# Kernel tuning notes

Hardware: AMD Instinct MI355X
Metric: run time of the kernel (lower is better)

The kernel has to match this reference:

```python
import jax, jax.numpy as jnp
import numpy as np

PAD = 1
K = 3  # kernel_size


def conv2d(x, w, b):
    y = jax.lax.conv_general_dilated(
        x, w, window_strides=(1, 1), padding=((PAD, PAD), (PAD, PAD)),
        dimension_numbers=("NCHW", "OIHW", "NCHW"))
    return y + b[None, :, None, None]


def deform_conv2d(x, offset, weight, bias):
    # torchvision.ops.deform_conv2d semantics (stride=1, dilation=1, 1 offset group)
    B, C, H, W = x.shape
    O = weight.shape[0]
    K2 = K * K
    off = offset.reshape(B, K2, 2, H, W)  # [...,0]=dy, [...,1]=dx
    ky, kx = jnp.meshgrid(jnp.arange(K), jnp.arange(K), indexing="ij")
    ky = ky.reshape(K2).astype(x.dtype)
    kx = kx.reshape(K2).astype(x.dtype)
    hh = jnp.arange(H, dtype=x.dtype)
    ww = jnp.arange(W, dtype=x.dtype)
    # sampling coords, shape [B, K2, H, W]
    py = off[:, :, 0] + ky[None, :, None, None] + hh[None, None, :, None] - PAD
    px = off[:, :, 1] + kx[None, :, None, None] + ww[None, None, None, :] - PAD

    y0 = jnp.floor(py)
    x0 = jnp.floor(px)
    wy = (py - y0)[:, None]  # [B,1,K2,H,W]
    wx = (px - x0)[:, None]

    xf = x.reshape(B, C, H * W)

    def gather(iy, ix):
        valid = (iy >= 0) & (iy < H) & (ix >= 0) & (ix < W)
        iyc = jnp.clip(iy, 0, H - 1).astype(jnp.int32)
        ixc = jnp.clip(ix, 0, W - 1).astype(jnp.int32)
        idx = (iyc * W + ixc).reshape(B, 1, K2 * H * W)
        v = jnp.take_along_axis(xf, idx, axis=2).reshape(B, C, K2, H, W)
        return v * valid.reshape(B, 1, K2, H, W).astype(x.dtype)

    v00 = gather(y0, x0)
    v01 = gather(y0, x0 + 1)
    v10 = gather(y0 + 1, x0)
    v11 = gather(y0 + 1, x0 + 1)
    sampled = (v00 * (1 - wy) * (1 - wx) + v01 * (1 - wy) * wx
               + v10 * wy * (1 - wx) + v11 * wy * wx)  # [B,C,K2,H,W]
    out = jnp.einsum("bckhw,ock->bohw", sampled, weight.reshape(O, C, K2))
    return out + bias[None, :, None, None]


def setup_inputs() -> dict:
    key = jax.random.key(0)
    k1, k2, k3, k4, k5 = jax.random.split(key, 5)
    B, C, H, W = 4, 64, 192, 192
    O = 64
    x = jax.random.normal(k1, (B, C, H, W), dtype=jnp.float32)
    w_off = jax.random.normal(k2, (2 * K * K, C, K, K), dtype=jnp.float32) * 0.05
    b_off = jnp.zeros((2 * K * K,), dtype=jnp.float32)
    w_conv = jax.random.normal(k3, (O, C, K, K), dtype=jnp.float32) * (1.0 / np.sqrt(C * K * K))
    b_conv = jax.random.normal(k4, (O,), dtype=jnp.float32) * 0.01
    return {"x": x, "w_off": w_off, "b_off": b_off, "w_conv": w_conv, "b_conv": b_conv}


def reference(x, w_off, b_off, w_conv, b_conv):
    offset = conv2d(x, w_off, b_off)
    y = deform_conv2d(x, offset, w_conv, b_conv)
    return conv2d(y, w_conv, b_conv)  # module reuses self.conv on deform output
```

## Files before the change

### kernel.cpp

```cpp
#include <hip/hip_runtime.h>

constexpr int B = 4;
constexpr int C = 64;
constexpr int O = 64;
constexpr int OOFF = 18;
constexpr int H = 192;
constexpr int W = 192;

typedef __attribute__((ext_vector_type(8))) short short8;
typedef __attribute__((ext_vector_type(4))) float float4v;
typedef __attribute__((ext_vector_type(2))) float f32x2;
typedef __attribute__((ext_vector_type(2))) uint u32x2;
typedef __attribute__((ext_vector_type(2))) __bf16 bf16x2;

__device__ inline ushort f2bf(float f) {
  return __builtin_bit_cast(ushort, (__bf16)f);
}
__device__ inline uint pk2bf(float lo, float hi) {
  bf16x2 v;
  v.x = (__bf16)lo;
  v.y = (__bf16)hi;
  return __builtin_bit_cast(uint, v);
}
__device__ inline f32x2 upk(uint u) {
  u32x2 t;
  t.x = u << 16;
  t.y = u & 0xffff0000u;
  return __builtin_bit_cast(f32x2, t);
}

__global__ __launch_bounds__(256) void k_pre(const float* __restrict__ x,
                                             ushort* __restrict__ xtb,
                                             const float* __restrict__ w_conv,
                                             ushort* __restrict__ wBf,
                                             const float* __restrict__ w_off,
                                             ushort* __restrict__ wOf) {
  __shared__ float tile[64][17];
  const int bid = blockIdx.x;
  const int tid = threadIdx.x;
  if (bid < 9216) {
    const int w0 = (bid % 12) * 16;
    const int h = (bid / 12) % 192;
    const int b = bid / 2304;
    const int wl = tid & 15;
    const int c0 = tid >> 4;
#pragma unroll
    for (int r = 0; r < 4; ++r) {
      const int c = c0 + r * 16;
      tile[c][wl] = x[(((size_t)b * C + c) * H + h) * W + w0 + wl];
    }
    __syncthreads();
    const int c = tid & 63;
    const int qq = tid >> 6;
#pragma unroll
    for (int r = 0; r < 4; ++r) {
      const int wq = qq + r * 4;
      xtb[(((size_t)b * H + h) * W + w0 + wq) * C + c] = f2bf(tile[c][wq]);
    }
  } else if (bid < 9360) {
    const int i = (bid - 9216) * 256 + tid;
    const int j = i & 7;
    const int lane = (i >> 3) & 63;
    const int nt = (i >> 9) & 3;
    const int kstep = (i >> 11) & 1;
    const int kk = i >> 12;
    const int n = nt + 4 * (lane & 15);
    const int c = kstep * 32 + ((lane >> 4) & 3) * 8 + j;
    wBf[i] = f2bf(w_conv[((size_t)n * C + c) * 9 + kk]);
  } else {
    const int i = (bid - 9360) * 256 + tid;
    const int j = i & 7;
    const int lane = (i >> 3) & 63;
    const int nt = (i >> 9) & 1;
    const int ks = (i >> 10) & 1;
    const int kk = i >> 11;
    const int n = nt * 16 + (lane & 15);
    const int c = ks * 32 + ((lane >> 4) & 3) * 8 + j;
    wOf[i] = (n < OOFF) ? f2bf(w_off[((size_t)n * C + c) * 9 + kk]) : (ushort)0;
  }
}

__global__ __launch_bounds__(128) void k_fused(
    const ushort* __restrict__ xtb, const ushort* __restrict__ wOf,
    const float* __restrict__ b_off, const ushort* __restrict__ wBf,
    const float* __restrict__ b_conv, ushort* __restrict__ yt) {
  __shared__ ushort sA[2][2][64][8];
  __shared__ __align__(16) float offBuf[2][16][20];

  const int bid = blockIdx.x;
  const int xcd = bid & 7;
  const int s0 = bid >> 3;
  const int b = xcd >> 1;
  const int half = xcd & 1;
  const int th = s0 / 24;
  const int tw = s0 % 24;

  const int tid = threadIdx.x;
  const int wave = tid >> 6, lane = tid & 63;
  const int h0 = half * 96 + th * 4 + wave * 2;
  const int w0 = tw * 8;

  const int col = lane & 15, quad = lane >> 4;
  const int p = lane >> 2, qtr = lane & 3;
  const int prow = p >> 3, pcol = p & 7;
  const int h = h0 + prow, w = w0 + pcol;

  {
    float4v oacc[2];
#pragma unroll
    for (int nt = 0; nt < 2; ++nt) oacc[nt] = (float4v){0.f, 0.f, 0.f, 0.f};

    short8 oafr[2][2];

    auto oload = [&](int kk, int pb) {
      const int ky = kk / 3, kx = kk % 3;
      const int hh = h0 + (col >> 3) + ky - 1;
      const int ww = w0 + (col & 7) + kx - 1;
      const bool ok = ((unsigned)hh < (unsigned)H) && ((unsigned)ww < (unsigned)W);
      const int hhc = min(max(hh, 0), H - 1);
      const int wwc = min(max(ww, 0), W - 1);
      const ushort* pa = xtb + (((size_t)b * H + hhc) * W + wwc) * C + quad * 8;
#pragma unroll
      for (int ks = 0; ks < 2; ++ks) {
        short8 v = (short8)0;
        if (ok) v = *(const short8*)(pa + ks * 32);
        oafr[pb][ks] = v;
      }
    };

    oload(0, 0);
#pragma unroll
    for (int kk = 0; kk < 9; ++kk) {
      const int pb = kk & 1;
      if (kk < 8) oload(kk + 1, pb ^ 1);
#pragma unroll
      for (int ks = 0; ks < 2; ++ks)
#pragma unroll
        for (int nt = 0; nt < 2; ++nt) {
          const short8 bw =
              *(const short8*)&wOf[((((size_t)kk * 2 + ks) * 2 + nt) * 64 + lane) * 8];
          oacc[nt] = __builtin_amdgcn_mfma_f32_16x16x32_bf16(oafr[pb][ks], bw, oacc[nt], 0, 0, 0);
        }
    }

#pragma unroll
    for (int nt = 0; nt < 2; ++nt) {
      const int oc = nt * 16 + col;
      if (oc < OOFF) {
        const float bias = b_off[oc];
#pragma unroll
        for (int r = 0; r < 4; ++r)
          offBuf[wave][quad * 4 + r][oc] = oacc[nt][r] + bias;
      }
    }
  }

  const ushort* xbase = xtb + (size_t)b * H * W * C;
  const uint qoff = (uint)qtr * 16u;
  const float hm1 = (float)(h - 1), wm1 = (float)(w - 1);

  uint offs[4];
  float4 awv;
  uint4 gA[4], gB[4];

  auto calc = [&](int kk) {
    const float2 ov = *(const float2*)&offBuf[wave][p][2 * kk];
    const int ky = kk / 3, kx = kk % 3;
    const float pyf = ov.x + hm1 + (float)ky;
    const float pxf = ov.y + wm1 + (float)kx;
    const float fy0 = floorf(pyf), fx0 = floorf(pxf);
    const float wy = pyf - fy0, wx = pxf - fx0;
    const int iy0 = (int)fy0, ix0 = (int)fx0;
    const int iy1 = iy0 + 1, ix1 = ix0 + 1;
    const bool vy0 = (unsigned)iy0 < (unsigned)H;
    const bool vy1 = (unsigned)iy1 < (unsigned)H;
    const bool vx0 = (unsigned)ix0 < (unsigned)W;
    const bool vx1 = (unsigned)ix1 < (unsigned)W;
    awv.x = (vy0 && vx0) ? (1.f - wy) * (1.f - wx) : 0.f;
    awv.y = (vy0 && vx1) ? (1.f - wy) * wx : 0.f;
    awv.z = (vy1 && vx0) ? wy * (1.f - wx) : 0.f;
    awv.w = (vy1 && vx1) ? wy * wx : 0.f;
    const int cy0 = min(max(iy0, 0), H - 1), cy1 = min(max(iy1, 0), H - 1);
    const int cx0 = min(max(ix0, 0), W - 1), cx1 = min(max(ix1, 0), W - 1);
    offs[0] = (uint)((cy0 * W + cx0) * (C * 2)) + qoff;
    offs[1] = (uint)((cy0 * W + cx1) * (C * 2)) + qoff;
    offs[2] = (uint)((cy1 * W + cx0) * (C * 2)) + qoff;
    offs[3] = (uint)((cy1 * W + cx1) * (C * 2)) + qoff;
  };

  auto loadAB = [&]() {
#pragma unroll
    for (int c = 0; c < 4; ++c)
      gA[c] = *(const uint4*)((const char*)xbase + offs[c]);
#pragma unroll
    for (int c = 0; c < 4; ++c)
      gB[c] = *(const uint4*)((const char*)xbase + offs[c] + 64u);
  };
  auto blend = [&](const uint4* g, uint* pk) {
    const f32x2 a00 = {awv.x, awv.x};
    const f32x2 a01 = {awv.y, awv.y};
    const f32x2 a10 = {awv.z, awv.z};
    const f32x2 a11 = {awv.w, awv.w};
#pragma unroll
    for (int i = 0; i < 4; ++i) {
      f32x2 sv = upk(g[0][i]) * a00 + upk(g[1][i]) * a01 + upk(g[2][i]) * a10 + upk(g[3][i]) * a11;
      pk[i] = pk2bf(sv.x, sv.y);
    }
  };

  float4v acc[4];
#pragma unroll
  for (int nt = 0; nt < 4; ++nt) acc[nt] = (float4v){0.f, 0.f, 0.f, 0.f};

  calc(0);
  loadAB();
#pragma unroll
  for (int kk = 0; kk < 9; ++kk) {
    uint pkA[4];
    blend(gA, pkA);
    *(uint4*)&sA[wave][0][p | (qtr << 4)][0] = *(const uint4*)pkA;
    uint pkB[4];
    blend(gB, pkB);
    *(uint4*)&sA[wave][1][p | (qtr << 4)][0] = *(const uint4*)pkB;

    if (kk < 8) {
      calc(kk + 1);
      loadAB();
    }

#pragma unroll
    for (int ks = 0; ks < 2; ++ks) {
      const short8 a = *(const short8*)&sA[wave][ks][lane][0];
#pragma unroll
      for (int nt = 0; nt < 4; ++nt) {
        const short8 bb = *(const short8*)&wBf[((((size_t)kk * 2 + ks) * 4 + nt) * 64 + lane) * 8];
        acc[nt] = __builtin_amdgcn_mfma_f32_16x16x32_bf16(a, bb, acc[nt], 0, 0, 0);
      }
    }
  }

  float bias[4];
#pragma unroll
  for (int nt = 0; nt < 4; ++nt) bias[nt] = b_conv[4 * col + nt];
#pragma unroll
  for (int r = 0; r < 4; ++r) {
    const int pp = quad * 4 + r;
    const int hrow = h0 + (pp >> 3), wcol = w0 + (pp & 7);
    uint2 u;
    u.x = pk2bf(acc[0][r] + bias[0], acc[1][r] + bias[1]);
    u.y = pk2bf(acc[2][r] + bias[2], acc[3][r] + bias[3]);
    *(uint2*)&yt[((size_t)(b * H + hrow) * W + wcol) * C + 4 * col] = u;
  }
}

__global__ __launch_bounds__(256) void k_conv_main_mfma(
    const ushort* __restrict__ yt, const ushort* __restrict__ wBf,
    const float* __restrict__ b_conv, float* __restrict__ out) {
  const int w0 = blockIdx.x * 16;
  const int b = blockIdx.z;
  const int tid = threadIdx.x;
  const int wave = tid >> 6, lane = tid & 63;
  const int col = lane & 15, quad = lane >> 4;
  const int h0 = blockIdx.y * 8 + wave * 2;

  float4v acc[2][4];
#pragma unroll
  for (int mt = 0; mt < 2; ++mt)
#pragma unroll
    for (int nt = 0; nt < 4; ++nt) acc[mt][nt] = (float4v){0.f, 0.f, 0.f, 0.f};

  short8 bfr[2][2][4];
  short8 afr[2][2][2];

  auto load = [&](int kk, int pb) {
    const int ky = kk / 3, kx = kk % 3;
    const int ww = w0 + col + kx - 1;
    const bool wok = (unsigned)ww < (unsigned)W;
    const int wwc = min(max(ww, 0), W - 1);
#pragma unroll
    for (int ks = 0; ks < 2; ++ks)
#pragma unroll
      for (int nt = 0; nt < 4; ++nt)
        bfr[pb][ks][nt] = *(const short8*)&wBf[((((size_t)kk * 2 + ks) * 4 + nt) * 64 + lane) * 8];
#pragma unroll
    for (int mt = 0; mt < 2; ++mt) {
      const int hh = h0 + mt + ky - 1;
      const bool ok = wok && ((unsigned)hh < (unsigned)H);
      const int hhc = min(max(hh, 0), H - 1);
      const ushort* pa = yt + (((size_t)b * H + hhc) * W + wwc) * C + quad * 8;
#pragma unroll
      for (int ks = 0; ks < 2; ++ks) {
        short8 v = (short8)0;
        if (ok) v = *(const short8*)(pa + ks * 32);
        afr[pb][mt][ks] = v;
      }
    }
  };

  load(0, 0);
#pragma unroll
  for (int kk = 0; kk < 9; ++kk) {
    const int pb = kk & 1;
    if (kk < 8) load(kk + 1, pb ^ 1);
#pragma unroll
    for (int ks = 0; ks < 2; ++ks)
#pragma unroll
      for (int mt = 0; mt < 2; ++mt)
#pragma unroll
        for (int nt = 0; nt < 4; ++nt)
          acc[mt][nt] = __builtin_amdgcn_mfma_f32_16x16x32_bf16(afr[pb][mt][ks], bfr[pb][ks][nt],
                                                                acc[mt][nt], 0, 0, 0);
  }

  float bias[4];
#pragma unroll
  for (int nt = 0; nt < 4; ++nt) bias[nt] = b_conv[4 * col + nt];
#pragma unroll
  for (int mt = 0; mt < 2; ++mt) {
    const int h = h0 + mt;
#pragma unroll
    for (int nt = 0; nt < 4; ++nt) {
      const int oc = 4 * col + nt;
      float4 v;
      v.x = acc[mt][nt][0] + bias[nt];
      v.y = acc[mt][nt][1] + bias[nt];
      v.z = acc[mt][nt][2] + bias[nt];
      v.w = acc[mt][nt][3] + bias[nt];
      *(float4*)&out[(((size_t)b * O + oc) * H + h) * W + w0 + quad * 4] = v;
    }
  }
}

extern "C" void kernel_launch(void* const* d_in, const int* in_sizes, int n_in,
                              void* d_out, int out_size, void* d_ws, size_t ws_size,
                              hipStream_t stream) {
  const float* x = (const float*)d_in[0];
  const float* w_off = (const float*)d_in[1];
  const float* b_off = (const float*)d_in[2];
  const float* w_conv = (const float*)d_in[3];
  const float* b_conv = (const float*)d_in[4];
  float* out = (float*)d_out;

  ushort* xtb = (ushort*)d_ws;
  ushort* yt = xtb + (size_t)B * H * W * C;
  ushort* wBf = yt + (size_t)B * H * W * C;
  ushort* wOf = wBf + 36864;

  k_pre<<<dim3(9432), dim3(256), 0, stream>>>(x, xtb, w_conv, wBf, w_off, wOf);
  k_fused<<<dim3(4608), dim3(128), 0, stream>>>(xtb, wOf, b_off, wBf, b_conv, yt);
  k_conv_main_mfma<<<dim3(W / 16, H / 8, B), dim3(256), 0, stream>>>(yt, wBf, b_conv, out);
}
```

Before: 200.1 us.

## Split offset conv into separate kernel with larger per-wave tiles

The offset-predicting convolution moves out of the fused deformable kernel into its own kernel. Each wave there computes four 16-pixel M-tiles, so every weight fragment load feeds four MFMAs. Offsets go to a global fp32 buffer (20-float stride per pixel) that the deform kernel reads with vector loads, replacing the shared-memory handoff. This adds a kernel launch and a global round trip for the offsets, but frees the deform kernel's registers and should improve its occupancy.

```diff
diff --git a/kernel.cpp b/kernel.cpp
--- a/kernel.cpp
+++ b/kernel.cpp
@@ -80,12 +80,88 @@
   }
 }
 
-__global__ __launch_bounds__(128) void k_fused(
-    const ushort* __restrict__ xtb, const ushort* __restrict__ wOf,
-    const float* __restrict__ b_off, const ushort* __restrict__ wBf,
-    const float* __restrict__ b_conv, ushort* __restrict__ yt) {
+__global__ __launch_bounds__(256) void k_offs(const ushort* __restrict__ xtb,
+                                              const ushort* __restrict__ wOf,
+                                              const float* __restrict__ b_off,
+                                              float* __restrict__ offp) {
+  const int tile = blockIdx.x * 4 + (threadIdx.x >> 6);
+  const int lane = threadIdx.x & 63;
+  const int xcd = tile & 7;
+  const int s0 = tile >> 3;
+  const int b = xcd >> 1;
+  const int half = xcd & 1;
+  const int th = s0 / 24;
+  const int tw = s0 % 24;
+  const int h0 = half * 96 + th * 8, w0 = tw * 8;
+  const int col = lane & 15, quad = lane >> 4;
+
+  float4v oacc[4][2];
+#pragma unroll
+  for (int mt = 0; mt < 4; ++mt)
+#pragma unroll
+    for (int nt = 0; nt < 2; ++nt) oacc[mt][nt] = (float4v){0.f, 0.f, 0.f, 0.f};
+
+  short8 oafr[2][4][2];
+
+  auto oload = [&](int kk, int pb) {
+    const int ky = kk / 3, kx = kk % 3;
+    const int ww = w0 + (col & 7) + kx - 1;
+    const bool wok = (unsigned)ww < (unsigned)W;
+    const int wwc = min(max(ww, 0), W - 1);
+#pragma unroll
+    for (int mt = 0; mt < 4; ++mt) {
+      const int hh = h0 + 2 * mt + (col >> 3) + ky - 1;
+      const bool ok = wok && ((unsigned)hh < (unsigned)H);
+      const int hhc = min(max(hh, 0), H - 1);
+      const ushort* pa = xtb + (((size_t)b * H + hhc) * W + wwc) * C + quad * 8;
+#pragma unroll
+      for (int ks = 0; ks < 2; ++ks) {
+        short8 v = (short8)0;
+        if (ok) v = *(const short8*)(pa + ks * 32);
+        oafr[pb][mt][ks] = v;
+      }
+    }
+  };
+
+  oload(0, 0);
+#pragma unroll 2
+  for (int kk = 0; kk < 9; ++kk) {
+    const int pb = kk & 1;
+    if (kk < 8) oload(kk + 1, pb ^ 1);
+#pragma unroll
+    for (int ks = 0; ks < 2; ++ks)
+#pragma unroll
+      for (int nt = 0; nt < 2; ++nt) {
+        const short8 bw = *(const short8*)&wOf[((((size_t)kk * 2 + ks) * 2 + nt) * 64 + lane) * 8];
+#pragma unroll
+        for (int mt = 0; mt < 4; ++mt)
+          oacc[mt][nt] =
+              __builtin_amdgcn_mfma_f32_16x16x32_bf16(oafr[pb][mt][ks], bw, oacc[mt][nt], 0, 0, 0);
+      }
+  }
+
+#pragma unroll
+  for (int nt = 0; nt < 2; ++nt) {
+    const int oc = nt * 16 + col;
+    if (oc < OOFF) {
+      const float bias = b_off[oc];
+#pragma unroll
+      for (int mt = 0; mt < 4; ++mt)
+#pragma unroll
+        for (int r = 0; r < 4; ++r) {
+          const int px = mt * 16 + quad * 4 + r;
+          const int hh = h0 + (px >> 3), ww = w0 + (px & 7);
+          offp[(((size_t)b * H + hh) * W + ww) * 20 + oc] = oacc[mt][nt][r] + bias;
+        }
+    }
+  }
+}
+
+__global__ __launch_bounds__(128) void k_deform(
+    const ushort* __restrict__ xtb, const float* __restrict__ offp,
+    const ushort* __restrict__ wBf, const float* __restrict__ b_conv,
+    ushort* __restrict__ yt) {
   __shared__ ushort sA[2][2][64][8];
-  __shared__ __align__(16) float offBuf[2][16][20];
 
   const int bid = blockIdx.x;
   const int xcd = bid & 7;
@@ -102,72 +178,33 @@
 
   const int col = lane & 15, quad = lane >> 4;
   const int p = lane >> 2, qtr = lane & 3;
-  const int prow = p >> 3, pcol = p & 7;
-  const int h = h0 + prow, w = w0 + pcol;
-
-  {
-    float4v oacc[2];
-#pragma unroll
-    for (int nt = 0; nt < 2; ++nt) oacc[nt] = (float4v){0.f, 0.f, 0.f, 0.f};
-
-    short8 oafr[2][2];
-
-    auto oload = [&](int kk, int pb) {
-      const int ky = kk / 3, kx = kk % 3;
-      const int hh = h0 + (col >> 3) + ky - 1;
-      const int ww = w0 + (col & 7) + kx - 1;
-      const bool ok = ((unsigned)hh < (unsigned)H) && ((unsigned)ww < (unsigned)W);
-      const int hhc = min(max(hh, 0), H - 1);
-      const int wwc = min(max(ww, 0), W - 1);
-      const ushort* pa = xtb + (((size_t)b * H + hhc) * W + wwc) * C + quad * 8;
-#pragma unroll
-      for (int ks = 0; ks < 2; ++ks) {
-        short8 v = (short8)0;
-        if (ok) v = *(const short8*)(pa + ks * 32);
-        oafr[pb][ks] = v;
-      }
-    };
-
-    oload(0, 0);
-#pragma unroll
-    for (int kk = 0; kk < 9; ++kk) {
-      const int pb = kk & 1;
-      if (kk < 8) oload(kk + 1, pb ^ 1);
-#pragma unroll
-      for (int ks = 0; ks < 2; ++ks)
-#pragma unroll
-        for (int nt = 0; nt < 2; ++nt) {
-          const short8 bw =
-              *(const short8*)&wOf[((((size_t)kk * 2 + ks) * 2 + nt) * 64 + lane) * 8];
-          oacc[nt] = __builtin_amdgcn_mfma_f32_16x16x32_bf16(oafr[pb][ks], bw, oacc[nt], 0, 0, 0);
-        }
-    }
-
-#pragma unroll
-    for (int nt = 0; nt < 2; ++nt) {
-      const int oc = nt * 16 + col;
-      if (oc < OOFF) {
-        const float bias = b_off[oc];
-#pragma unroll
-        for (int r = 0; r < 4; ++r)
-          offBuf[wave][quad * 4 + r][oc] = oacc[nt][r] + bias;
-      }
-    }
-  }
+  const int ph = h0 + (p >> 3), pw = w0 + (p & 7);
+
+  const float* orow = offp + (((size_t)b * H + ph) * W + pw) * 20;
+  const float4 v0 = *(const float4*)(orow + 0);
+  const float4 v1 = *(const float4*)(orow + 4);
+  const float4 v2 = *(const float4*)(orow + 8);
+  const float4 v3 = *(const float4*)(orow + 12);
+  const float2 v4 = *(const float2*)(orow + 16);
+  float oy[9], ox[9];
+  oy[0] = v0.x; ox[0] = v0.y; oy[1] = v0.z; ox[1] = v0.w;
+  oy[2] = v1.x; ox[2] = v1.y; oy[3] = v1.z; ox[3] = v1.w;
+  oy[4] = v2.x; ox[4] = v2.y; oy[5] = v2.z; ox[5] = v2.w;
+  oy[6] = v3.x; ox[6] = v3.y; oy[7] = v3.z; ox[7] = v3.w;
+  oy[8] = v4.x; ox[8] = v4.y;
 
   const ushort* xbase = xtb + (size_t)b * H * W * C;
   const uint qoff = (uint)qtr * 16u;
-  const float hm1 = (float)(h - 1), wm1 = (float)(w - 1);
+  const float hm1 = (float)(ph - 1), wm1 = (float)(pw - 1);
 
   uint offs[4];
   float4 awv;
   uint4 gA[4], gB[4];
 
   auto calc = [&](int kk) {
-    const float2 ov = *(const float2*)&offBuf[wave][p][2 * kk];
     const int ky = kk / 3, kx = kk % 3;
-    const float pyf = ov.x + hm1 + (float)ky;
-    const float pxf = ov.y + wm1 + (float)kx;
+    const float pyf = oy[kk] + hm1 + (float)ky;
+    const float pxf = ox[kk] + wm1 + (float)kx;
     const float fy0 = floorf(pyf), fx0 = floorf(pxf);
     const float wy = pyf - fy0, wx = pxf - fx0;
     const int iy0 = (int)fy0, ix0 = (int)fx0;
@@ -345,8 +382,10 @@
   ushort* yt = xtb + (size_t)B * H * W * C;
   ushort* wBf = yt + (size_t)B * H * W * C;
   ushort* wOf = wBf + 36864;
+  float* offp = (float*)(wOf + 18432);
 
   k_pre<<<dim3(9432), dim3(256), 0, stream>>>(x, xtb, w_conv, wBf, w_off, wOf);
-  k_fused<<<dim3(4608), dim3(128), 0, stream>>>(xtb, wOf, b_off, wBf, b_conv, yt);
+  k_offs<<<dim3(576), dim3(256), 0, stream>>>(xtb, wOf, b_off, offp);
+  k_deform<<<dim3(4608), dim3(128), 0, stream>>>(xtb, offp, wBf, b_conv, yt);
   k_conv_main_mfma<<<dim3(W / 16, H / 8, B), dim3(256), 0, stream>>>(yt, wBf, b_conv, out);
 }
```

Measured after the change: 211.5 us. 1.06x slower.
